# Kernel optimization log

Measured on AMD Instinct MI355X. Metric: run time of the kernel, lower is better.

The kernel has to match this reference:

```python
import jax, jax.numpy as jnp
import numpy as np

B, S, H = 2, 2048, 2048
NH, NKV, D = 16, 4, 128
E, K, F = 16, 2, 768
EPS = 1e-6
THETA = 1e6


def setup_inputs() -> dict:
    key = jax.random.key(0)
    ks = jax.random.split(key, 10)
    sd = 0.02
    rn = lambda k, shp: jax.random.normal(k, shp, jnp.float32) * sd
    return {
        "positions": jnp.arange(S, dtype=jnp.int32),
        "hidden_states": jax.random.normal(ks[0], (B, S, H), jnp.float32),
        "residual": jax.random.normal(ks[1], (B, S, H), jnp.float32),
        "w_in_ln": jnp.ones((H,), jnp.float32),
        "wq": rn(ks[2], (H, NH * D)),
        "wk": rn(ks[3], (H, NKV * D)),
        "wv": rn(ks[4], (H, NKV * D)),
        "wo": rn(ks[5], (NH * D, H)),
        "q_norm_w": jnp.ones((D,), jnp.float32),
        "k_norm_w": jnp.ones((D,), jnp.float32),
        "w_post_ln": jnp.ones((H,), jnp.float32),
        "gate_w": rn(ks[6], (H, E)),
        "w_gate_up": rn(ks[7], (E, H, 2 * F)),
        "w_down": rn(ks[8], (E, F, H)),
    }


def _rmsnorm(x, w):
    return x * jax.lax.rsqrt(jnp.mean(x * x, axis=-1, keepdims=True) + EPS) * w


def _rope(x, positions):
    # x: [B, S, h, D], neox-style rotate-half RoPE
    half = D // 2
    inv_freq = 1.0 / (THETA ** (jnp.arange(half, dtype=jnp.float32) / half))
    ang = positions.astype(jnp.float32)[:, None] * inv_freq  # [S, half]
    cos = jnp.cos(ang)[None, :, None, :]
    sin = jnp.sin(ang)[None, :, None, :]
    x1, x2 = x[..., :half], x[..., half:]
    return jnp.concatenate([x1 * cos - x2 * sin, x2 * cos + x1 * sin], axis=-1)


def reference(positions, hidden_states, residual, w_in_ln, wq, wk, wv, wo,
              q_norm_w, k_norm_w, w_post_ln, gate_w, w_gate_up, w_down):
    # fused RMSNorm + residual (residual is not None branch)
    residual = hidden_states + residual
    h = _rmsnorm(residual, w_in_ln)

    # --- Qwen3 attention: qk-norm + RoPE + causal GQA ---
    q = _rmsnorm((h @ wq).reshape(B, S, NH, D), q_norm_w)
    k = _rmsnorm((h @ wk).reshape(B, S, NKV, D), k_norm_w)
    v = (h @ wv).reshape(B, S, NKV, D)
    q = _rope(q, positions)
    k = _rope(k, positions)
    rep = NH // NKV
    k = jnp.repeat(k, rep, axis=2)
    v = jnp.repeat(v, rep, axis=2)
    scores = jnp.einsum('bqhd,bkhd->bhqk', q, k) / np.sqrt(D).astype(np.float32)
    causal = jnp.tril(jnp.ones((S, S), bool))
    scores = jnp.where(causal, scores, -jnp.inf)
    attn = jax.nn.softmax(scores, axis=-1)
    o = jnp.einsum('bhqk,bkhd->bqhd', attn, v).reshape(B, S, NH * D) @ wo

    # fused RMSNorm + residual
    residual = o + residual
    h = _rmsnorm(residual, w_post_ln)

    # --- MoE: top-k router (renormalized) + capacity-based grouped GEMM dispatch ---
    x = h.reshape(-1, H)                      # [T, H]
    T = B * S
    probs = jax.nn.softmax((x @ gate_w).astype(jnp.float32), axis=-1)
    tw, tids = jax.lax.top_k(probs, K)        # [T, K]
    tw = (tw / tw.sum(axis=-1, keepdims=True)).astype(x.dtype)

    P = T * K
    C = (2 * P) // E
    eids = tids.reshape(-1)                   # [P]
    oneh = jax.nn.one_hot(eids, E, dtype=jnp.int32)
    pos_in_e = (jnp.cumsum(oneh, axis=0) * oneh).sum(-1) - 1   # slot within expert
    valid = pos_in_e < C
    pos_c = jnp.minimum(pos_in_e, C - 1)
    e_safe = jnp.where(valid, eids, E)        # overflow -> dump row E

    xr = jnp.repeat(x, K, axis=0)             # [P, H]
    buf = jnp.zeros((E + 1, C, H), x.dtype).at[e_safe, pos_c].set(xr)[:E]
    gu = jnp.einsum('ech,ehf->ecf', buf, w_gate_up)            # [E, C, 2F]
    g, u = jnp.split(gu, 2, axis=-1)
    dn = jnp.einsum('ecf,efh->ech', jax.nn.silu(g) * u, w_down)
    dn = jnp.concatenate([dn, jnp.zeros((1, C, H), dn.dtype)], axis=0)
    yp = dn[e_safe, pos_c] * tw.reshape(-1)[:, None]           # [P, H]
    y = yp.reshape(T, K, H).sum(axis=1)
    return y.reshape(B, S, H), residual
```

## Files before the change

### kernel.cpp

```cpp
#include <hip/hip_runtime.h>
#include <stdint.h>

#define T_TOK 4096
#define HDIM  2048
#define SEQ   2048
#define NHQ   16
#define NKVH  4
#define DH    128
#define NE    16
#define CCAP  1024
#define FF    768
#define EPSF  1e-6f

typedef __attribute__((ext_vector_type(4))) float          f32x4;
typedef __attribute__((ext_vector_type(8))) _Float16       f16x8;
typedef __attribute__((ext_vector_type(4))) unsigned short u16x4;
typedef __attribute__((ext_vector_type(8))) unsigned short u16x8;

__device__ __forceinline__ unsigned short f2h(float f){ return __builtin_bit_cast(unsigned short, (_Float16)f); }
__device__ __forceinline__ float h2f(unsigned short u){ return (float)__builtin_bit_cast(_Float16, u); }
__device__ __forceinline__ void split2(float x, unsigned short& hi, unsigned short& lo){
  unsigned short h = f2h(x);
  hi = h; lo = f2h((x - h2f(h)) * 4096.f);
}
__device__ __forceinline__ void gl_lds16(const void* g, void* l){
  __builtin_amdgcn_global_load_lds((const __attribute__((address_space(1))) unsigned int*)g,
                                   (__attribute__((address_space(3))) unsigned int*)l, 16, 0, 0);
}
__device__ __forceinline__ int bswz(int row){ return ((row & 7) ^ ((row >> 3) & 7)) << 3; }

__global__ __launch_bounds__(256) void k_addnorm(
    const float* __restrict__ hs, const float* __restrict__ rs, const float* __restrict__ w,
    float* __restrict__ resid, unsigned short* __restrict__ hhi, unsigned short* __restrict__ hlo)
{
  int t = blockIdx.x, tid = threadIdx.x;
  size_t off = (size_t)t * HDIM;
  float4 a0 = ((const float4*)(hs+off))[tid];
  float4 b0 = ((const float4*)(rs+off))[tid];
  float4 a1 = ((const float4*)(hs+off))[tid+256];
  float4 b1 = ((const float4*)(rs+off))[tid+256];
  float4 s0 = make_float4(a0.x+b0.x, a0.y+b0.y, a0.z+b0.z, a0.w+b0.w);
  float4 s1 = make_float4(a1.x+b1.x, a1.y+b1.y, a1.z+b1.z, a1.w+b1.w);
  float ssq = s0.x*s0.x+s0.y*s0.y+s0.z*s0.z+s0.w*s0.w
            + s1.x*s1.x+s1.y*s1.y+s1.z*s1.z+s1.w*s1.w;
  #pragma unroll
  for (int sh=1; sh<64; sh<<=1) ssq += __shfl_xor(ssq, sh);
  __shared__ float red[4];
  if ((tid & 63) == 0) red[tid>>6] = ssq;
  __syncthreads();
  float tot = red[0]+red[1]+red[2]+red[3];
  float r = 1.f / sqrtf(tot * (1.f/HDIM) + EPSF);
  ((float4*)(resid+off))[tid]     = s0;
  ((float4*)(resid+off))[tid+256] = s1;
  float4 w0 = ((const float4*)w)[tid];
  float4 w1 = ((const float4*)w)[tid+256];
  u16x4 hv, lv; unsigned short ta, tb;
  split2(s0.x*r*w0.x, ta, tb); hv.x=ta; lv.x=tb;
  split2(s0.y*r*w0.y, ta, tb); hv.y=ta; lv.y=tb;
  split2(s0.z*r*w0.z, ta, tb); hv.z=ta; lv.z=tb;
  split2(s0.w*r*w0.w, ta, tb); hv.w=ta; lv.w=tb;
  ((u16x4*)(hhi+off))[tid] = hv; ((u16x4*)(hlo+off))[tid] = lv;
  split2(s1.x*r*w1.x, ta, tb); hv.x=ta; lv.x=tb;
  split2(s1.y*r*w1.y, ta, tb); hv.y=ta; lv.y=tb;
  split2(s1.z*r*w1.z, ta, tb); hv.z=ta; lv.z=tb;
  split2(s1.w*r*w1.w, ta, tb); hv.w=ta; lv.w=tb;
  ((u16x4*)(hhi+off))[tid+256] = hv; ((u16x4*)(hlo+off))[tid+256] = lv;
}

__global__ void k_cstab(const int* __restrict__ pos, float* __restrict__ cs)
{
  int i = blockIdx.x*256 + threadIdx.x;
  if (i >= SEQ*64) return;
  int s = i >> 6, f = i & 63;
  float pw  = (float)exp((double)f * 13.815510557964274 / 64.0);
  float inv = 1.0f / pw;
  float ang = (float)pos[s] * inv;
  float sv, cv;
  sincosf(ang, &sv, &cv);
  ((float2*)cs)[i] = make_float2(cv, sv);
}

__global__ __launch_bounds__(256) void k_normrope(
    unsigned short* __restrict__ qh, unsigned short* __restrict__ ql,
    unsigned short* __restrict__ kh, unsigned short* __restrict__ kl,
    const float* __restrict__ qnw, const float* __restrict__ knw,
    const float* __restrict__ cs)
{
  int t = blockIdx.x, head = blockIdx.y*4 + (threadIdx.x>>6), lane = threadIdx.x & 63;
  int s = t & (SEQ-1);
  unsigned short *dh, *dl; const float* wn; float scale; size_t off;
  if (head < NHQ){ off = ((size_t)t*NHQ + head)*DH; dh = qh+off; dl = ql+off; wn = qnw; scale = 0.08838834764831845f; }
  else           { off = ((size_t)t*NKVH + (head-NHQ))*DH; dh = kh+off; dl = kl+off; wn = knw; scale = 1.f; }
  float x1 = h2f(dh[lane])    + h2f(dl[lane])   *(1.f/4096.f);
  float x2 = h2f(dh[lane+64]) + h2f(dl[lane+64])*(1.f/4096.f);
  float ssq = x1*x1 + x2*x2;
  #pragma unroll
  for (int sh=1; sh<64; sh<<=1) ssq += __shfl_xor(ssq, sh);
  float r = 1.f / sqrtf(ssq * (1.f/DH) + EPSF);
  float y1 = x1*r*wn[lane], y2 = x2*r*wn[lane+64];
  float2 csp = ((const float2*)cs)[s*64 + lane];
  float o1 = (y1*csp.x - y2*csp.y) * scale;
  float o2 = (y2*csp.x + y1*csp.y) * scale;
  unsigned short a, b;
  split2(o1, a, b); dh[lane]    = a; dl[lane]    = b;
  split2(o2, a, b); dh[lane+64] = a; dl[lane+64] = b;
}

__global__ __launch_bounds__(256) void k_wsplit(
    const float* __restrict__ W, int Kd, int Ncols,
    unsigned short* __restrict__ Whi, unsigned short* __restrict__ Wlo)
{
  int k0 = blockIdx.x*64, n0 = blockIdx.y*64;
  __shared__ float T[64][65];
  int tid = threadIdx.x;
  int tr = tid >> 4;
  int tc = (tid & 15) * 4;
  #pragma unroll
  for (int i=0;i<4;i++){
    int k = tr + i*16;
    float4 v = *(const float4*)(W + (size_t)(k0 + k)*Ncols + n0 + tc);
    T[k][tc+0]=v.x; T[k][tc+1]=v.y; T[k][tc+2]=v.z; T[k][tc+3]=v.w;
  }
  __syncthreads();
  int n  = tid >> 2;
  int kc = (tid & 3) * 16;
  u16x8 hv0, lv0, hv1, lv1;
  #pragma unroll
  for (int j=0;j<8;j++){
    unsigned short hi, lo; split2(T[kc+j][n], hi, lo);
    hv0[j]=hi; lv0[j]=lo;
  }
  #pragma unroll
  for (int j=0;j<8;j++){
    unsigned short hi, lo; split2(T[kc+8+j][n], hi, lo);
    hv1[j]=hi; lv1[j]=lo;
  }
  size_t ob = (size_t)(n0 + n)*Kd + k0 + kc;
  *(u16x8*)(Whi + ob)     = hv0;
  *(u16x8*)(Whi + ob + 8) = hv1;
  *(u16x8*)(Wlo + ob)     = lv0;
  *(u16x8*)(Wlo + ob + 8) = lv1;
}

__global__ __launch_bounds__(256,2) void k_gemm_qkv(
    const unsigned short* __restrict__ Ahi, const unsigned short* __restrict__ Alo,
    const unsigned short* __restrict__ Whi, const unsigned short* __restrict__ Wlo,
    unsigned short* __restrict__ qh, unsigned short* __restrict__ ql,
    unsigned short* __restrict__ kh, unsigned short* __restrict__ kl,
    unsigned short* __restrict__ vh, unsigned short* __restrict__ vl)
{
  const int Kd = HDIM;
  int bm = blockIdx.x, bn2 = blockIdx.y;
  int bn, N, noff; unsigned short *Ch, *Cl;
  if (bn2 < 16){ bn = bn2;      N = 2048; noff = 0;    Ch = qh; Cl = ql; }
  else if (bn2 < 20){ bn = bn2-16; N = 512; noff = 2048; Ch = kh; Cl = kl; }
  else { bn = bn2-20; N = 512; noff = 2560; Ch = vh; Cl = vl; }

  __shared__ unsigned short As[2][8192];
  __shared__ unsigned short Bs[2][8192];

  int tid = threadIdx.x, lane = tid & 63, w = tid >> 6;
  int wr = w >> 1, wc = w & 1;

  size_t arow_g[4], brow_g[4];
  int lb_[4];
  #pragma unroll
  for (int i=0;i<4;i++){
    int ob = w*4096 + i*1024 + lane*16;
    int row = ob >> 7;
    int colB = ob & 127;
    int scolB = colB ^ ((row & 7) << 4);
    arow_g[i] = (size_t)(bm*128 + row) * Kd + (scolB >> 1);
    brow_g[i] = (size_t)(noff + bn*128 + row) * Kd + (scolB >> 1);
    lb_[i] = (w*4096 + i*1024) >> 1;
  }

  f32x4 accA[4][4] = {};
  f32x4 accB[4][4] = {};

  for (int kt = 0; kt < Kd/64; kt++){
    #pragma unroll
    for (int i=0;i<4;i++){
      gl_lds16(Ahi + arow_g[i] + kt*64, (void*)&As[0][lb_[i]]);
      gl_lds16(Alo + arow_g[i] + kt*64, (void*)&As[1][lb_[i]]);
      gl_lds16(Whi + brow_g[i] + kt*64, (void*)&Bs[0][lb_[i]]);
      gl_lds16(Wlo + brow_g[i] + kt*64, (void*)&Bs[1][lb_[i]]);
    }
    __syncthreads();
    #pragma unroll
    for (int kk=0; kk<2; kk++){
      f16x8 ah[4], al[4], bh[4], bl[4];
      #pragma unroll
      for (int m=0;m<4;m++){
        int row = wr*64 + m*16 + (lane & 15);
        int ci = (kk*32 + ((lane>>4)<<3)) ^ ((row & 7) << 3);
        ah[m] = *(const f16x8*)&As[0][row*64 + ci];
        al[m] = *(const f16x8*)&As[1][row*64 + ci];
      }
      #pragma unroll
      for (int n=0;n<4;n++){
        int row = wc*64 + n*16 + (lane & 15);
        int ci = (kk*32 + ((lane>>4)<<3)) ^ ((row & 7) << 3);
        bh[n] = *(const f16x8*)&Bs[0][row*64 + ci];
        bl[n] = *(const f16x8*)&Bs[1][row*64 + ci];
      }
      #pragma unroll
      for (int m=0;m<4;m++)
        #pragma unroll
        for (int n=0;n<4;n++){
          accA[m][n] = __builtin_amdgcn_mfma_f32_16x16x32_f16(ah[m], bh[n], accA[m][n], 0,0,0);
          accB[m][n] = __builtin_amdgcn_mfma_f32_16x16x32_f16(ah[m], bl[n], accB[m][n], 0,0,0);
          accB[m][n] = __builtin_amdgcn_mfma_f32_16x16x32_f16(al[m], bh[n], accB[m][n], 0,0,0);
        }
    }
    __syncthreads();
  }
  int r0 = (lane >> 4) << 2, c0 = lane & 15;
  #pragma unroll
  for (int m=0;m<4;m++){
    int grow0 = bm*128 + wr*64 + m*16 + r0;
    #pragma unroll
    for (int n=0;n<4;n++){
      int gcol = bn*128 + wc*64 + n*16 + c0;
      #pragma unroll
      for (int j=0;j<4;j++){
        float v = accA[m][n][j] + accB[m][n][j] * (1.f/4096.f);
        int grow = grow0 + j;
        unsigned short hi, lo; split2(v, hi, lo);
        Ch[(size_t)grow*N + gcol] = hi;
        Cl[(size_t)grow*N + gcol] = lo;
      }
    }
  }
}

__global__ __launch_bounds__(256,2) void k_gemm_o(
    const unsigned short* __restrict__ Ahi, const unsigned short* __restrict__ Alo,
    const unsigned short* __restrict__ Bhi, const unsigned short* __restrict__ Blo,
    float* __restrict__ C1)
{
  const int Kd = HDIM, N = 2048;
  int bm = blockIdx.x, bn = blockIdx.y;

  __shared__ unsigned short As[2][8192];
  __shared__ unsigned short Bs[2][8192];

  int tid = threadIdx.x, lane = tid & 63, w = tid >> 6;
  int wr = w >> 1, wc = w & 1;

  size_t arow_g[4], brow_g[4];
  int lb_[4];
  #pragma unroll
  for (int i=0;i<4;i++){
    int ob = w*4096 + i*1024 + lane*16;
    int row = ob >> 7;
    int colB = ob & 127;
    int scolB = colB ^ ((row & 7) << 4);
    arow_g[i] = (size_t)(bm*128 + row) * Kd + (scolB >> 1);
    brow_g[i] = (size_t)(bn*128 + row) * Kd + (scolB >> 1);
    lb_[i] = (w*4096 + i*1024) >> 1;
  }

  f32x4 accA[4][4] = {};
  f32x4 accB[4][4] = {};

  for (int kt = 0; kt < Kd/64; kt++){
    #pragma unroll
    for (int i=0;i<4;i++){
      gl_lds16(Ahi + arow_g[i] + kt*64, (void*)&As[0][lb_[i]]);
      gl_lds16(Alo + arow_g[i] + kt*64, (void*)&As[1][lb_[i]]);
      gl_lds16(Bhi + brow_g[i] + kt*64, (void*)&Bs[0][lb_[i]]);
      gl_lds16(Blo + brow_g[i] + kt*64, (void*)&Bs[1][lb_[i]]);
    }
    __syncthreads();
    #pragma unroll
    for (int kk=0; kk<2; kk++){
      f16x8 ah[4], al[4], bh[4], bl[4];
      #pragma unroll
      for (int m=0;m<4;m++){
        int row = wr*64 + m*16 + (lane & 15);
        int ci = (kk*32 + ((lane>>4)<<3)) ^ ((row & 7) << 3);
        ah[m] = *(const f16x8*)&As[0][row*64 + ci];
        al[m] = *(const f16x8*)&As[1][row*64 + ci];
      }
      #pragma unroll
      for (int n=0;n<4;n++){
        int row = wc*64 + n*16 + (lane & 15);
        int ci = (kk*32 + ((lane>>4)<<3)) ^ ((row & 7) << 3);
        bh[n] = *(const f16x8*)&Bs[0][row*64 + ci];
        bl[n] = *(const f16x8*)&Bs[1][row*64 + ci];
      }
      #pragma unroll
      for (int m=0;m<4;m++)
        #pragma unroll
        for (int n=0;n<4;n++){
          accA[m][n] = __builtin_amdgcn_mfma_f32_16x16x32_f16(ah[m], bh[n], accA[m][n], 0,0,0);
          accB[m][n] = __builtin_amdgcn_mfma_f32_16x16x32_f16(ah[m], bl[n], accB[m][n], 0,0,0);
          accB[m][n] = __builtin_amdgcn_mfma_f32_16x16x32_f16(al[m], bh[n], accB[m][n], 0,0,0);
        }
    }
    __syncthreads();
  }
  int r0 = (lane >> 4) << 2, c0 = lane & 15;
  #pragma unroll
  for (int m=0;m<4;m++){
    int grow0 = bm*128 + wr*64 + m*16 + r0;
    #pragma unroll
    for (int n=0;n<4;n++){
      int gcol = bn*128 + wc*64 + n*16 + c0;
      #pragma unroll
      for (int j=0;j<4;j++){
        float v = accA[m][n][j] + accB[m][n][j] * (1.f/4096.f);
        int grow = grow0 + j;
        C1[(size_t)grow*N + gcol] += v;
      }
    }
  }
}

__global__ __launch_bounds__(256,2) void k_gemm_down(
    const unsigned short* __restrict__ Aact,
    const float* __restrict__ Bsrc,
    float* __restrict__ yp,
    const int* __restrict__ erow, const int* __restrict__ counts)
{
  const int Kd = FF, N = HDIM;
  int bn = blockIdx.x, e = blockIdx.y, bm = blockIdx.z;
  int cnt = counts[e]; if (bm*128 >= cnt) return;
  const float* Bp = Bsrc + (size_t)e*Kd*N;
  const unsigned short* Abase = Aact + (size_t)e*CCAP*Kd;

  __shared__ unsigned short As[8192];
  __shared__ unsigned short Bs[8192];

  int tid = threadIdx.x, lane = tid & 63, w = tid >> 6;
  int wr = w >> 1, wc = w & 1;

  size_t arow_g[4];
  int lb_[4];
  #pragma unroll
  for (int i=0;i<4;i++){
    int ob = w*4096 + i*1024 + lane*16;
    int row = ob >> 7;
    int colB = ob & 127;
    int scolB = colB ^ ((row & 7) << 4);
    int grow = bm*128 + row;
    arow_g[i] = (size_t)grow * Kd + (scolB >> 1);
    lb_[i] = (w*4096 + i*1024) >> 1;
  }

  f32x4 accA[4][4] = {};

  int nK = Kd >> 6;
  for (int kt = 0; kt < nK; kt++){
    #pragma unroll
    for (int i=0;i<4;i++)
      gl_lds16(Abase + arow_g[i] + kt*64, (void*)&As[lb_[i]]);
    #pragma unroll
    for (int it=0; it<2; it++){
      int b2 = tid + it*256;
      int k0 = (b2 >> 5) << 2;
      int n0 = (b2 & 31) << 2;
      const float* bp = Bp + (size_t)(kt*64 + k0)*N + bn*128 + n0;
      float4 f0 = *(const float4*)bp;
      float4 f1 = *(const float4*)(bp + (size_t)N);
      float4 f2 = *(const float4*)(bp + 2*(size_t)N);
      float4 f3 = *(const float4*)(bp + 3*(size_t)N);
      #define DO_COL(J, CX) { \
        int rown = n0 + J; \
        int idx = rown*64 + (k0 ^ bswz(rown)); \
        u16x4 ph; ph.x=f2h(f0.CX); ph.y=f2h(f1.CX); ph.z=f2h(f2.CX); ph.w=f2h(f3.CX); \
        *(u16x4*)&Bs[idx] = ph; }
      DO_COL(0, x) DO_COL(1, y) DO_COL(2, z) DO_COL(3, w)
      #undef DO_COL
    }
    __syncthreads();
    #pragma unroll
    for (int kk=0; kk<2; kk++){
      f16x8 ah[4], bh[4];
      #pragma unroll
      for (int m=0;m<4;m++){
        int row = wr*64 + m*16 + (lane & 15);
        int ci = (kk*32 + ((lane>>4)<<3)) ^ ((row & 7) << 3);
        ah[m] = *(const f16x8*)&As[row*64 + ci];
      }
      #pragma unroll
      for (int n=0;n<4;n++){
        int row = wc*64 + n*16 + (lane & 15);
        int ci = (kk*32 + ((lane>>4)<<3)) ^ bswz(row);
        bh[n] = *(const f16x8*)&Bs[row*64 + ci];
      }
      #pragma unroll
      for (int m=0;m<4;m++)
        #pragma unroll
        for (int n=0;n<4;n++)
          accA[m][n] = __builtin_amdgcn_mfma_f32_16x16x32_f16(ah[m], bh[n], accA[m][n], 0,0,0);
    }
    __syncthreads();
  }
  int r0 = (lane >> 4) << 2, c0 = lane & 15;
  #pragma unroll
  for (int m=0;m<4;m++){
    int grow0 = bm*128 + wr*64 + m*16 + r0;
    #pragma unroll
    for (int n=0;n<4;n++){
      int gcol = bn*128 + wc*64 + n*16 + c0;
      #pragma unroll
      for (int j=0;j<4;j++){
        int grow = grow0 + j;
        if (grow < cnt){
          int p = erow[e*CCAP + grow];
          yp[(size_t)p*N + gcol] = accA[m][n][j];
        }
      }
    }
  }
}

__global__ __launch_bounds__(256,2) void k_gemm_gu(
    const unsigned short* __restrict__ Ahi,
    const float* __restrict__ Bsrc,
    unsigned short* __restrict__ act,
    const int* __restrict__ erow, const int* __restrict__ counts)
{
  const int Kd = HDIM, N = 1536;
  int bn = blockIdx.x, e = blockIdx.y, bm = blockIdx.z;
  int cnt = counts[e]; if (bm*128 >= cnt) return;
  const float* Bp = Bsrc + (size_t)e*Kd*N;

  __shared__ unsigned short As [8192];
  __shared__ unsigned short BsG[8192];
  __shared__ unsigned short BsU[8192];

  int tid = threadIdx.x, lane = tid & 63, w = tid >> 6;
  int wr = w >> 1, wc = w & 1;

  size_t arow_g[4];
  int lb_[4];
  #pragma unroll
  for (int i=0;i<4;i++){
    int ob = w*4096 + i*1024 + lane*16;
    int row = ob >> 7;
    int colB = ob & 127;
    int scolB = colB ^ ((row & 7) << 4);
    int grow = erow[e*CCAP + bm*128 + row] >> 1;
    arow_g[i] = (size_t)grow * Kd + (scolB >> 1);
    lb_[i] = (w*4096 + i*1024) >> 1;
  }

  f32x4 accG[4][4] = {};
  f32x4 accU[4][4] = {};

  for (int kt = 0; kt < Kd/64; kt++){
    #pragma unroll
    for (int i=0;i<4;i++)
      gl_lds16(Ahi + arow_g[i] + kt*64, (void*)&As[lb_[i]]);
    #pragma unroll
    for (int it=0; it<2; it++){
      int b2 = tid + it*256;
      int k0 = (b2 >> 5) << 2;
      int n0 = (b2 & 31) << 2;
      const float* bpg = Bp + (size_t)(kt*64 + k0)*N + bn*128 + n0;
      const float* bpu = bpg + 768;
      float4 g0 = *(const float4*)bpg;
      float4 g1 = *(const float4*)(bpg + (size_t)N);
      float4 g2 = *(const float4*)(bpg + 2*(size_t)N);
      float4 g3 = *(const float4*)(bpg + 3*(size_t)N);
      float4 u0 = *(const float4*)bpu;
      float4 u1 = *(const float4*)(bpu + (size_t)N);
      float4 u2 = *(const float4*)(bpu + 2*(size_t)N);
      float4 u3 = *(const float4*)(bpu + 3*(size_t)N);
      #define DO_COL2(J, CX) { \
        int rown = n0 + J; \
        int idx = rown*64 + (k0 ^ bswz(rown)); \
        u16x4 pg; pg.x=f2h(g0.CX); pg.y=f2h(g1.CX); pg.z=f2h(g2.CX); pg.w=f2h(g3.CX); \
        *(u16x4*)&BsG[idx] = pg; \
        u16x4 pu; pu.x=f2h(u0.CX); pu.y=f2h(u1.CX); pu.z=f2h(u2.CX); pu.w=f2h(u3.CX); \
        *(u16x4*)&BsU[idx] = pu; }
      DO_COL2(0, x) DO_COL2(1, y) DO_COL2(2, z) DO_COL2(3, w)
      #undef DO_COL2
    }
    __syncthreads();
    #pragma unroll
    for (int kk=0; kk<2; kk++){
      f16x8 ah[4], bg[4], bu[4];
      #pragma unroll
      for (int m=0;m<4;m++){
        int row = wr*64 + m*16 + (lane & 15);
        int ci = (kk*32 + ((lane>>4)<<3)) ^ ((row & 7) << 3);
        ah[m] = *(const f16x8*)&As[row*64 + ci];
      }
      #pragma unroll
      for (int n=0;n<4;n++){
        int row = wc*64 + n*16 + (lane & 15);
        int ci = (kk*32 + ((lane>>4)<<3)) ^ bswz(row);
        bg[n] = *(const f16x8*)&BsG[row*64 + ci];
        bu[n] = *(const f16x8*)&BsU[row*64 + ci];
      }
      #pragma unroll
      for (int m=0;m<4;m++)
        #pragma unroll
        for (int n=0;n<4;n++){
          accG[m][n] = __builtin_amdgcn_mfma_f32_16x16x32_f16(ah[m], bg[n], accG[m][n], 0,0,0);
          accU[m][n] = __builtin_amdgcn_mfma_f32_16x16x32_f16(ah[m], bu[n], accU[m][n], 0,0,0);
        }
    }
    __syncthreads();
  }
  int r0 = (lane >> 4) << 2, c0 = lane & 15;
  #pragma unroll
  for (int m=0;m<4;m++){
    int grow0 = bm*128 + wr*64 + m*16 + r0;
    #pragma unroll
    for (int n=0;n<4;n++){
      int gcol = bn*128 + wc*64 + n*16 + c0;
      #pragma unroll
      for (int j=0;j<4;j++){
        int grow = grow0 + j;
        unsigned short g16 = f2h(accG[m][n][j]);
        unsigned short u16_ = f2h(accU[m][n][j]);
        float gf = h2f(g16), uf = h2f(u16_);
        float s = gf / (1.f + __expf(-gf));
        act[((size_t)e*CCAP + grow)*FF + gcol] = f2h(s * uf);
      }
    }
  }
}

__global__ __launch_bounds__(512,2) void k_attn(
    const unsigned short* __restrict__ qh, const unsigned short* __restrict__ ql,
    const unsigned short* __restrict__ kh, const unsigned short* __restrict__ kl,
    const unsigned short* __restrict__ vh, const unsigned short* __restrict__ vl,
    unsigned short* __restrict__ oh, unsigned short* __restrict__ ol)
{
  int h = blockIdx.y, b = blockIdx.z;
  int qt = b ? (15 - blockIdx.x) : blockIdx.x;
  int hkv = h >> 2;
  int tid = threadIdx.x, lane = tid & 63, w = tid >> 6;

  __shared__ unsigned short Ks[2][2][8192];
  __shared__ unsigned short Vs[2][2][8192];
  __shared__ unsigned short Ps[8][2][1024];

  int qrow = qt*128 + w*16 + (lane & 15);
  size_t qoff = ((size_t)(b*SEQ + qrow)*NHQ + h)*DH + ((lane>>4)<<3);
  f16x8 qfh[4], qfl[4];
  #pragma unroll
  for (int kk=0; kk<4; kk++){
    qfh[kk] = *(const f16x8*)(qh + qoff + kk*32);
    qfl[kk] = *(const f16x8*)(ql + qoff + kk*32);
  }

  const size_t SROW = (size_t)NKVH*DH;
  size_t kvbase = (size_t)b*SEQ*SROW + (size_t)hkv*DH;
  int kob[2]; size_t koff[2];
  #pragma unroll
  for (int i=0;i<2;i++){
    int ob = i*8192 + tid*16;
    int row = ob >> 8;
    int scol = (ob & 255) ^ ((row & 7) << 4);
    kob[i] = ob;
    koff[i] = (size_t)row*SROW + (scol >> 1);
  }
  int vkvp = (tid & 31) * 2;
  int vd0  = ((tid >> 5) & 15) * 8;
  size_t voff0 = (size_t)vkvp*SROW + vd0;
  size_t voff1 = voff0 + SROW;

  u16x8 pkh[2], pkl[2];
  u16x8 pvh[2], pvl[2];

  #define STAGE_LOAD(KVT) { \
    size_t tb = kvbase + (size_t)(KVT)*64*SROW; \
    _Pragma("unroll") \
    for (int i=0;i<2;i++){ pkh[i] = *(const u16x8*)(kh + tb + koff[i]); \
                           pkl[i] = *(const u16x8*)(kl + tb + koff[i]); } \
    pvh[0] = *(const u16x8*)(vh + tb + voff0); \
    pvh[1] = *(const u16x8*)(vh + tb + voff1); \
    pvl[0] = *(const u16x8*)(vl + tb + voff0); \
    pvl[1] = *(const u16x8*)(vl + tb + voff1); }

  #define STAGE_WRITE(BUF) { \
    _Pragma("unroll") \
    for (int i=0;i<2;i++){ \
      *(u16x8*)((char*)&Ks[BUF][0][0] + kob[i]) = pkh[i]; \
      *(u16x8*)((char*)&Ks[BUF][1][0] + kob[i]) = pkl[i]; } \
    _Pragma("unroll") \
    for (int jj=0;jj<8;jj++){ \
      int row = vd0 + jj; \
      int idx = row*64 + (vkvp ^ ((jj & 7) << 3)); \
      *(unsigned int*)&Vs[BUF][0][idx] = (unsigned int)pvh[0][jj] | ((unsigned int)pvh[1][jj] << 16); \
      *(unsigned int*)&Vs[BUF][1][idx] = (unsigned int)pvl[0][jj] | ((unsigned int)pvl[1][jj] << 16); } }

  #define QKT(KVT, BUF) { \
    f32x4 saA[4] = {}; \
    f32x4 saB[4] = {}; \
    __builtin_amdgcn_s_setprio(1); \
    _Pragma("unroll") \
    for (int kk=0; kk<4; kk++){ \
      _Pragma("unroll") \
      for (int n=0;n<4;n++){ \
        int row = n*16 + (lane & 15); \
        int ci = (kk*32 + ((lane>>4)<<3)) ^ ((row & 7) << 3); \
        f16x8 kfh = *(const f16x8*)&Ks[BUF][0][row*128 + ci]; \
        f16x8 kfl = *(const f16x8*)&Ks[BUF][1][row*128 + ci]; \
        saA[n] = __builtin_amdgcn_mfma_f32_16x16x32_f16(qfh[kk], kfh, saA[n], 0,0,0); \
        saB[n] = __builtin_amdgcn_mfma_f32_16x16x32_f16(qfh[kk], kfl, saB[n], 0,0,0); \
        saB[n] = __builtin_amdgcn_mfma_f32_16x16x32_f16(qfl[kk], kfh, saB[n], 0,0,0); } } \
    __builtin_amdgcn_s_setprio(0); \
    _Pragma("unroll") \
    for (int j=0;j<4;j++) mx[j] = -1e30f; \
    int qg = qt*128 + w*16 + ((lane>>4)<<2); \
    _Pragma("unroll") \
    for (int n=0;n<4;n++){ \
      int kvcol = (KVT)*64 + n*16 + (lane & 15); \
      _Pragma("unroll") \
      for (int j=0;j<4;j++){ \
        float sv = saA[n][j] + saB[n][j]*(1.f/4096.f); \
        if (kvcol > qg + j) sv = -1e30f; \
        p[n][j] = sv; \
        mx[j] = fmaxf(mx[j], sv); } } }

  #define SOFTMAX() { \
    _Pragma("unroll") \
    for (int sh=1; sh<16; sh<<=1) \
      _Pragma("unroll") \
      for (int j=0;j<4;j++) mx[j] = fmaxf(mx[j], __shfl_xor(mx[j], sh)); \
    float rs[4], sum[4]; \
    _Pragma("unroll") \
    for (int j=0;j<4;j++){ \
      float mn = fmaxf(m_[j], mx[j]); \
      rs[j] = __expf(m_[j] - mn); \
      float sm = 0.f; \
      _Pragma("unroll") \
      for (int n=0;n<4;n++){ float pe = __expf(p[n][j] - mn); p[n][j] = pe; sm += pe; } \
      sum[j] = sm; \
      m_[j] = mn; } \
    _Pragma("unroll") \
    for (int sh=1; sh<16; sh<<=1) \
      _Pragma("unroll") \
      for (int j=0;j<4;j++) sum[j] += __shfl_xor(sum[j], sh); \
    _Pragma("unroll") \
    for (int j=0;j<4;j++) l_[j] = l_[j]*rs[j] + sum[j]; \
    _Pragma("unroll") \
    for (int d=0;d<8;d++) \
      _Pragma("unroll") \
      for (int j=0;j<4;j++){ oaccA[d][j] *= rs[j]; oaccB[d][j] *= rs[j]; } \
    _Pragma("unroll") \
    for (int n=0;n<4;n++) \
      _Pragma("unroll") \
      for (int j=0;j<4;j++){ \
        int r = ((lane>>4)<<2) + j; \
        int c = n*16 + (lane & 15); \
        int idx = r*64 + (c ^ ((r & 7) << 3)); \
        unsigned short ph, pl2; split2(p[n][j], ph, pl2); \
        Ps[w][0][idx] = ph; \
        Ps[w][1][idx] = pl2; } }

  #define PVOP(BUF) { \
    __builtin_amdgcn_s_setprio(1); \
    _Pragma("unroll") \
    for (int kk=0; kk<2; kk++){ \
      int prow = lane & 15; \
      int pidx = prow*64 + ((kk*32 + ((lane>>4)<<3)) ^ ((prow & 7) << 3)); \
      f16x8 pah = *(const f16x8*)&Ps[w][0][pidx]; \
      f16x8 pal = *(const f16x8*)&Ps[w][1][pidx]; \
      _Pragma("unroll") \
      for (int d=0;d<8;d++){ \
        int row = d*16 + (lane & 15); \
        int ci = (kk*32 + ((lane>>4)<<3)) ^ ((row & 7) << 3); \
        f16x8 vfh = *(const f16x8*)&Vs[BUF][0][row*64 + ci]; \
        f16x8 vfl = *(const f16x8*)&Vs[BUF][1][row*64 + ci]; \
        oaccA[d] = __builtin_amdgcn_mfma_f32_16x16x32_f16(pah, vfh, oaccA[d], 0,0,0); \
        oaccB[d] = __builtin_amdgcn_mfma_f32_16x16x32_f16(pah, vfl, oaccB[d], 0,0,0); \
        oaccB[d] = __builtin_amdgcn_mfma_f32_16x16x32_f16(pal, vfh, oaccB[d], 0,0,0); } } \
    __builtin_amdgcn_s_setprio(0); }

  float m_[4], l_[4];
  f32x4 oaccA[8] = {};
  f32x4 oaccB[8] = {};
  #pragma unroll
  for (int j=0;j<4;j++){ m_[j] = -1e30f; l_[j] = 0.f; }

  int nkt = 2*qt + 2;
  STAGE_LOAD(0); STAGE_WRITE(0);
  STAGE_LOAD(1); STAGE_WRITE(1);
  __syncthreads();

  float p[4][4], mx[4];
  QKT(0, 0);

  for (int kvt = 0; kvt < nkt; kvt++){
    int cur = kvt & 1, nxt = cur ^ 1;
    if (kvt+2 < nkt) STAGE_LOAD(kvt+2);

    bool active = (kvt*64 <= qt*128 + w*16 + 15);
    bool actn   = (kvt+1 < nkt) && ((kvt+1)*64 <= qt*128 + w*16 + 15);
    if (actn){
      SOFTMAX();
      QKT(kvt+1, nxt);
      PVOP(cur);
    } else if (active){
      SOFTMAX();
      PVOP(cur);
    }
    __syncthreads();
    if (kvt+2 < nkt) STAGE_WRITE(cur);
    __syncthreads();
  }
  #undef STAGE_LOAD
  #undef STAGE_WRITE
  #undef QKT
  #undef SOFTMAX
  #undef PVOP

  #pragma unroll
  for (int j=0;j<4;j++) l_[j] = 1.f / l_[j];
  #pragma unroll
  for (int d=0;d<8;d++)
    #pragma unroll
    for (int j=0;j<4;j++){
      int qr = qt*128 + w*16 + ((lane>>4)<<2) + j;
      size_t off = ((size_t)(b*SEQ + qr)*NHQ + h)*DH + d*16 + (lane & 15);
      float v = (oaccA[d][j] + oaccB[d][j]*(1.f/4096.f)) * l_[j];
      unsigned short hi, lo; split2(v, hi, lo);
      oh[off] = hi; ol[off] = lo;
    }
}

__global__ __launch_bounds__(256) void k_ln2gate(
    const float* __restrict__ resid, const float* __restrict__ wln,
    const float* __restrict__ gw,
    unsigned short* __restrict__ x2, float* __restrict__ topw, int* __restrict__ topid)
{
  int t = blockIdx.x, tid = threadIdx.x;
  size_t off = (size_t)t * HDIM;
  float4 s0 = ((const float4*)(resid+off))[tid];
  float4 s1 = ((const float4*)(resid+off))[tid+256];
  float ssq = s0.x*s0.x+s0.y*s0.y+s0.z*s0.z+s0.w*s0.w
            + s1.x*s1.x+s1.y*s1.y+s1.z*s1.z+s1.w*s1.w;
  #pragma unroll
  for (int sh=1; sh<64; sh<<=1) ssq += __shfl_xor(ssq, sh);
  __shared__ float red[4];
  if ((tid & 63) == 0) red[tid>>6] = ssq;
  __syncthreads();
  float tot = red[0]+red[1]+red[2]+red[3];
  float r = 1.f / sqrtf(tot * (1.f/HDIM) + EPSF);
  float4 w0 = ((const float4*)wln)[tid];
  float4 w1 = ((const float4*)wln)[tid+256];
  float xs[8] = { s0.x*r*w0.x, s0.y*r*w0.y, s0.z*r*w0.z, s0.w*r*w0.w,
                  s1.x*r*w1.x, s1.y*r*w1.y, s1.z*r*w1.z, s1.w*r*w1.w };
  u16x4 hv;
  hv.x = f2h(xs[0]); hv.y = f2h(xs[1]); hv.z = f2h(xs[2]); hv.w = f2h(xs[3]);
  ((u16x4*)(x2+off))[tid] = hv;
  hv.x = f2h(xs[4]); hv.y = f2h(xs[5]); hv.z = f2h(xs[6]); hv.w = f2h(xs[7]);
  ((u16x4*)(x2+off))[tid+256] = hv;

  double acc[16];
  #pragma unroll
  for (int e2=0;e2<16;e2++) acc[e2] = 0.0;
  #pragma unroll
  for (int i=0;i<8;i++){
    int hidx = (i<4) ? (tid*4 + i) : (1024 + tid*4 + (i-4));
    const float4* g4 = (const float4*)(gw + (size_t)hidx*NE);
    float4 ga=g4[0], gb=g4[1], gc=g4[2], gd=g4[3];
    double xx = (double)xs[i];
    acc[0]+=xx*ga.x;  acc[1]+=xx*ga.y;  acc[2]+=xx*ga.z;  acc[3]+=xx*ga.w;
    acc[4]+=xx*gb.x;  acc[5]+=xx*gb.y;  acc[6]+=xx*gb.z;  acc[7]+=xx*gb.w;
    acc[8]+=xx*gc.x;  acc[9]+=xx*gc.y;  acc[10]+=xx*gc.z; acc[11]+=xx*gc.w;
    acc[12]+=xx*gd.x; acc[13]+=xx*gd.y; acc[14]+=xx*gd.z; acc[15]+=xx*gd.w;
  }
  __shared__ double red2[256][16];
  #pragma unroll
  for (int e2=0;e2<16;e2++) red2[tid][e2] = acc[e2];
  __syncthreads();
  for (int s=128; s>=1; s>>=1){
    if (tid < s){
      #pragma unroll
      for (int e2=0;e2<16;e2++) red2[tid][e2] += red2[tid+s][e2];
    }
    __syncthreads();
  }
  if (tid == 0){
    float l[16];
    #pragma unroll
    for (int e2=0;e2<16;e2++) l[e2] = (float)red2[0][e2];
    int i0 = 0;
    #pragma unroll
    for (int e2=1;e2<16;e2++) if (l[e2] > l[i0]) i0 = e2;
    int i1 = (i0 == 0) ? 1 : 0;
    #pragma unroll
    for (int e2=0;e2<16;e2++) if (e2 != i0 && l[e2] > l[i1]) i1 = e2;
    float w0t = 1.f / (1.f + expf(l[i1] - l[i0]));
    topw[t*2+0] = w0t; topw[t*2+1] = 1.f - w0t;
    topid[t*2+0] = i0; topid[t*2+1] = i1;
  }
}

__global__ __launch_bounds__(256) void k_route(
    int* __restrict__ topid, int* __restrict__ erow, int* __restrict__ counts)
{
  int tid = threadIdx.x;
  __shared__ unsigned short cnt[256][16];
  for (int i = tid; i < NE*CCAP; i += 256) erow[i] = 0;
  int loc[16];
  #pragma unroll
  for (int e2=0;e2<16;e2++) loc[e2] = 0;
  int myid[32];
  for (int i=0;i<32;i++){
    int e2 = topid[tid*32 + i];
    myid[i] = e2;
    loc[e2]++;
  }
  #pragma unroll
  for (int e2=0;e2<16;e2++) cnt[tid][e2] = (unsigned short)loc[e2];
  __syncthreads();
  if (tid < 16){
    int run = 0;
    for (int i=0;i<256;i++){ int c = cnt[i][tid]; cnt[i][tid] = (unsigned short)run; run += c; }
    counts[tid] = run > CCAP ? CCAP : run;
  }
  __syncthreads();
  #pragma unroll
  for (int e2=0;e2<16;e2++) loc[e2] = cnt[tid][e2];
  for (int i=0;i<32;i++){
    int e2 = myid[i];
    int pos = loc[e2]++;
    int p = tid*32 + i;
    int ok = (pos < CCAP);
    if (ok) erow[e2*CCAP + pos] = p;
    topid[p] = ok;
  }
}

__global__ __launch_bounds__(256) void k_gather(
    const float* __restrict__ yp, const int* __restrict__ valid,
    const float* __restrict__ topw, float* __restrict__ y)
{
  int t = blockIdx.x, tid = threadIdx.x;
  int v0 = valid[t*2+0], v1 = valid[t*2+1];
  float w0 = topw[t*2+0], w1 = topw[t*2+1];
  size_t o = (size_t)t*2*HDIM;
  const float4* r0 = (const float4*)(yp + o);
  const float4* r1 = (const float4*)(yp + o + HDIM);
  float4* yo = (float4*)(y + (size_t)t*HDIM);
  #pragma unroll
  for (int i=0;i<2;i++){
    int ix = tid + i*256;
    float4 a = r0[ix];
    float4 b = r1[ix];
    float4 out;
    float a0 = v0 ? w0 : 0.f;
    float b0 = v1 ? w1 : 0.f;
    out.x = (v0 ? a.x*a0 : 0.f) + (v1 ? b.x*b0 : 0.f);
    out.y = (v0 ? a.y*a0 : 0.f) + (v1 ? b.y*b0 : 0.f);
    out.z = (v0 ? a.z*a0 : 0.f) + (v1 ? b.z*b0 : 0.f);
    out.w = (v0 ? a.w*a0 : 0.f) + (v1 ? b.w*b0 : 0.f);
    yo[ix] = out;
  }
}

extern "C" void kernel_launch(void* const* d_in, const int* in_sizes, int n_in,
                              void* d_out, int out_size, void* d_ws, size_t ws_size,
                              hipStream_t stream)
{
  (void)in_sizes; (void)n_in; (void)out_size; (void)ws_size;
  const int*   positions = (const int*)  d_in[0];
  const float* hs        = (const float*)d_in[1];
  const float* res       = (const float*)d_in[2];
  const float* w_in_ln   = (const float*)d_in[3];
  const float* wq        = (const float*)d_in[4];
  const float* wk        = (const float*)d_in[5];
  const float* wv        = (const float*)d_in[6];
  const float* wo        = (const float*)d_in[7];
  const float* q_norm_w  = (const float*)d_in[8];
  const float* k_norm_w  = (const float*)d_in[9];
  const float* w_post_ln = (const float*)d_in[10];
  const float* gate_w    = (const float*)d_in[11];
  const float* w_gate_up = (const float*)d_in[12];
  const float* w_down    = (const float*)d_in[13];

  float* y      = (float*)d_out;
  float* resid2 = y + (size_t)T_TOK*HDIM;

  char* ws = (char*)d_ws;
  unsigned short* hhi = (unsigned short*)(ws + 0);
  unsigned short* hlo = (unsigned short*)(ws + 16777216);
  unsigned short* qh  = (unsigned short*)(ws + 33554432);
  unsigned short* ql  = (unsigned short*)(ws + 50331648);
  unsigned short* kh  = (unsigned short*)(ws + 67108864);
  unsigned short* kl  = (unsigned short*)(ws + 71303168);
  unsigned short* vh  = (unsigned short*)(ws + 75497472);
  unsigned short* vl  = (unsigned short*)(ws + 79691776);
  unsigned short* oh  = (unsigned short*)(ws + 83886080);
  unsigned short* ol  = (unsigned short*)(ws + 100663296);
  unsigned short* x2  = (unsigned short*)(ws + 117440512);
  unsigned short* qkvwh = (unsigned short*)(ws + 83886080);
  unsigned short* qkvwl = (unsigned short*)(ws + 96468992);
  unsigned short* wowh  = (unsigned short*)(ws + 117440512);
  unsigned short* wowl  = (unsigned short*)(ws + 125829120);
  unsigned short* act = (unsigned short*)(ws + 67108864);
  float*          yp  = (float*)         (ws + 0);
  float* cstab        = (float*)(ws + 134217728);
  float* topw         = (float*)(ws + 135266304);
  int*   topid        = (int*)  (ws + 135299072);
  int*   counts       = (int*)  (ws + 135331840);
  int*   erow         = (int*)  (ws + 135332096);

  k_addnorm<<<T_TOK, 256, 0, stream>>>(hs, res, w_in_ln, resid2, hhi, hlo);
  k_cstab<<<(SEQ*64 + 255)/256, 256, 0, stream>>>(positions, cstab);
  k_wsplit<<<dim3(32, 32), 256, 0, stream>>>(wq, HDIM, 2048, qkvwh,                     qkvwl);
  k_wsplit<<<dim3(32,  8), 256, 0, stream>>>(wk, HDIM,  512, qkvwh + (size_t)2048*HDIM, qkvwl + (size_t)2048*HDIM);
  k_wsplit<<<dim3(32,  8), 256, 0, stream>>>(wv, HDIM,  512, qkvwh + (size_t)2560*HDIM, qkvwl + (size_t)2560*HDIM);
  k_wsplit<<<dim3(32, 32), 256, 0, stream>>>(wo, HDIM, 2048, wowh,                      wowl);
  k_gemm_qkv<<<dim3(32,24,1), 256, 0, stream>>>(hhi, hlo, qkvwh, qkvwl, qh, ql, kh, kl, vh, vl);
  k_normrope<<<dim3(T_TOK, 5), 256, 0, stream>>>(qh, ql, kh, kl, q_norm_w, k_norm_w, cstab);
  k_attn<<<dim3(16, 16, 2), 512, 0, stream>>>(qh, ql, kh, kl, vh, vl, oh, ol);
  k_gemm_o<<<dim3(32,16,1), 256, 0, stream>>>(oh, ol, wowh, wowl, resid2);
  k_ln2gate<<<T_TOK, 256, 0, stream>>>(resid2, w_post_ln, gate_w, x2, topw, topid);
  k_route<<<1, 256, 0, stream>>>(topid, erow, counts);
  k_gemm_gu<<<dim3(6,16,8), 256, 0, stream>>>(x2, w_gate_up, act, erow, counts);
  k_gemm_down<<<dim3(16,16,8), 256, 0, stream>>>(act, w_down, yp, erow, counts);
  k_gather<<<T_TOK, 256, 0, stream>>>(yp, topid, topw, y);
}
```

Measured before the change: 842.7 us.

## Merge QKV weight-split launches, XCD-aware O-proj tiles, shuffle gate reduction

Replaces the three separate q/k/v weight split launches with one kernel whose grid covers all three matrices, removing two launches and their tail effects. Remaps k_gemm_o block indices so blocks that land on the same XCD work on neighbouring 8x8 tiles, aiming for better L2 reuse of A and B panels. Replaces the shared-memory tree reduction in the router gate with wave shuffles plus a four-way final sum, cutting barriers and LDS traffic. The double-precision summation order changes, which could flip near-tied top-k choices.

After: 868.2 us. 3.0% more time.

```diff
diff --git a/kernel.cpp b/kernel.cpp
--- a/kernel.cpp
+++ b/kernel.cpp
@@ -142,6 +142,47 @@
   *(u16x8*)(Wlo + ob + 8) = lv1;
 }
 
+__global__ __launch_bounds__(256) void k_wsplit3(
+    const float* __restrict__ wq, const float* __restrict__ wk, const float* __restrict__ wv,
+    unsigned short* __restrict__ Whi, unsigned short* __restrict__ Wlo)
+{
+  const int Kd = HDIM;
+  int k0 = blockIdx.x*64, ny = blockIdx.y;
+  const float* W; int Ncols, n0, noff;
+  if (ny < 32){ W = wq; Ncols = 2048; n0 = ny*64;      noff = 0;    }
+  else if (ny < 40){ W = wk; Ncols = 512; n0 = (ny-32)*64; noff = 2048; }
+  else { W = wv; Ncols = 512; n0 = (ny-40)*64; noff = 2560; }
+  __shared__ float T[64][65];
+  int tid = threadIdx.x;
+  int tr = tid >> 4;
+  int tc = (tid & 15) * 4;
+  #pragma unroll
+  for (int i=0;i<4;i++){
+    int k = tr + i*16;
+    float4 v = *(const float4*)(W + (size_t)(k0 + k)*Ncols + n0 + tc);
+    T[k][tc+0]=v.x; T[k][tc+1]=v.y; T[k][tc+2]=v.z; T[k][tc+3]=v.w;
+  }
+  __syncthreads();
+  int n  = tid >> 2;
+  int kc = (tid & 3) * 16;
+  u16x8 hv0, lv0, hv1, lv1;
+  #pragma unroll
+  for (int j=0;j<8;j++){
+    unsigned short hi, lo; split2(T[kc+j][n], hi, lo);
+    hv0[j]=hi; lv0[j]=lo;
+  }
+  #pragma unroll
+  for (int j=0;j<8;j++){
+    unsigned short hi, lo; split2(T[kc+8+j][n], hi, lo);
+    hv1[j]=hi; lv1[j]=lo;
+  }
+  size_t ob = (size_t)(noff + n0 + n)*Kd + k0 + kc;
+  *(u16x8*)(Whi + ob)     = hv0;
+  *(u16x8*)(Whi + ob + 8) = hv1;
+  *(u16x8*)(Wlo + ob)     = lv0;
+  *(u16x8*)(Wlo + ob + 8) = lv1;
+}
+
 __global__ __launch_bounds__(256,2) void k_gemm_qkv(
     const unsigned short* __restrict__ Ahi, const unsigned short* __restrict__ Alo,
     const unsigned short* __restrict__ Whi, const unsigned short* __restrict__ Wlo,
@@ -240,7 +281,10 @@
     float* __restrict__ C1)
 {
   const int Kd = HDIM, N = 2048;
-  int bm = blockIdx.x, bn = blockIdx.y;
+  int id = blockIdx.x + 32*blockIdx.y;
+  int xcd = id & 7, rr = id >> 3;
+  int bm = ((xcd & 3) << 3) + (rr & 7);
+  int bn = ((xcd >> 2) << 3) + (rr >> 3);
 
   __shared__ unsigned short As[2][8192];
   __shared__ unsigned short Bs[2][8192];
@@ -770,21 +814,21 @@
     acc[8]+=xx*gc.x;  acc[9]+=xx*gc.y;  acc[10]+=xx*gc.z; acc[11]+=xx*gc.w;
     acc[12]+=xx*gd.x; acc[13]+=xx*gd.y; acc[14]+=xx*gd.z; acc[15]+=xx*gd.w;
   }
-  __shared__ double red2[256][16];
-  #pragma unroll
-  for (int e2=0;e2<16;e2++) red2[tid][e2] = acc[e2];
+  #pragma unroll
+  for (int sh=1; sh<64; sh<<=1)
+    #pragma unroll
+    for (int e2=0;e2<16;e2++) acc[e2] += __shfl_xor(acc[e2], sh);
+  __shared__ double red2[4][16];
+  if ((tid & 63) == 0){
+    #pragma unroll
+    for (int e2=0;e2<16;e2++) red2[tid>>6][e2] = acc[e2];
+  }
   __syncthreads();
-  for (int s=128; s>=1; s>>=1){
-    if (tid < s){
-      #pragma unroll
-      for (int e2=0;e2<16;e2++) red2[tid][e2] += red2[tid+s][e2];
-    }
-    __syncthreads();
-  }
   if (tid == 0){
     float l[16];
     #pragma unroll
-    for (int e2=0;e2<16;e2++) l[e2] = (float)red2[0][e2];
+    for (int e2=0;e2<16;e2++)
+      l[e2] = (float)(red2[0][e2] + red2[1][e2] + red2[2][e2] + red2[3][e2]);
     int i0 = 0;
     #pragma unroll
     for (int e2=1;e2<16;e2++) if (l[e2] > l[i0]) i0 = e2;
@@ -909,10 +953,8 @@
 
   k_addnorm<<<T_TOK, 256, 0, stream>>>(hs, res, w_in_ln, resid2, hhi, hlo);
   k_cstab<<<(SEQ*64 + 255)/256, 256, 0, stream>>>(positions, cstab);
-  k_wsplit<<<dim3(32, 32), 256, 0, stream>>>(wq, HDIM, 2048, qkvwh,                     qkvwl);
-  k_wsplit<<<dim3(32,  8), 256, 0, stream>>>(wk, HDIM,  512, qkvwh + (size_t)2048*HDIM, qkvwl + (size_t)2048*HDIM);
-  k_wsplit<<<dim3(32,  8), 256, 0, stream>>>(wv, HDIM,  512, qkvwh + (size_t)2560*HDIM, qkvwl + (size_t)2560*HDIM);
-  k_wsplit<<<dim3(32, 32), 256, 0, stream>>>(wo, HDIM, 2048, wowh,                      wowl);
+  k_wsplit3<<<dim3(32, 48), 256, 0, stream>>>(wq, wk, wv, qkvwh, qkvwl);
+  k_wsplit<<<dim3(32, 32), 256, 0, stream>>>(wo, HDIM, 2048, wowh, wowl);
   k_gemm_qkv<<<dim3(32,24,1), 256, 0, stream>>>(hhi, hlo, qkvwh, qkvwl, qh, ql, kh, kl, vh, vl);
   k_normrope<<<dim3(T_TOK, 5), 256, 0, stream>>>(qh, ql, kh, kl, q_norm_w, k_norm_w, cstab);
   k_attn<<<dim3(16, 16, 2), 512, 0, stream>>>(qh, ql, kh, kl, vh, vl, oh, ol);
```
